# Performance work log

Measured on AMD Instinct MI355X. Metric: run time of the kernel, lower is better.

## Reference

```python
import jax, jax.numpy as jnp
import numpy as np

N = 20000   # nodes per graph
E = 320000  # edges per graph
D_IN, D_H = 128, 304


def _param(key, shape, fan_in):
    return jax.random.normal(key, shape, dtype=jnp.float32) / np.sqrt(fan_in)


def setup_inputs() -> dict:
    key = jax.random.key(0)
    ks = jax.random.split(key, 20)
    inp = {}
    for i, name in enumerate(['x1', 'x2', 'x3']):
        inp[name] = jax.random.normal(ks[i], (N, D_IN), dtype=jnp.float32)
    for i, name in enumerate(['src1', 'dst1', 'src2', 'dst2', 'src3', 'dst3']):
        inp[name] = jax.random.randint(ks[3 + i], (E,), 0, N, dtype=jnp.int32)
    # shared GraphConv weights (DGL GraphConv: h = norm_agg(x) @ W + b)
    inp['W1'] = _param(ks[9], (D_IN, D_H), D_IN)
    inp['b1'] = jnp.zeros((D_H,), jnp.float32)
    inp['W2'] = _param(ks[10], (D_H, D_H), D_H)
    inp['b2'] = jnp.zeros((D_H,), jnp.float32)
    inp['W3'] = _param(ks[11], (D_H, D_H), D_H)
    inp['b3'] = jnp.zeros((D_H,), jnp.float32)
    # MLP head: 304 -> 128 -> 64 -> 1
    inp['fW1'] = _param(ks[12], (D_H, 128), D_H)
    inp['fb1'] = jnp.zeros((128,), jnp.float32)
    inp['fW2'] = _param(ks[13], (128, 64), 128)
    inp['fb2'] = jnp.zeros((64,), jnp.float32)
    inp['fW3'] = _param(ks[14], (64, 1), 64)
    inp['fb3'] = jnp.zeros((1,), jnp.float32)
    return inp


def gcn_conv(x, src, dst, W, b):
    # DGL GraphConv, norm='both': h = D_in^{-1/2} A D_out^{-1/2} x W + b
    ones = jnp.ones((src.shape[0],), x.dtype)
    out_deg = jnp.clip(jax.ops.segment_sum(ones, src, num_segments=N), 1.0)
    in_deg = jnp.clip(jax.ops.segment_sum(ones, dst, num_segments=N), 1.0)
    h = x * jax.lax.rsqrt(out_deg)[:, None]
    agg = jax.ops.segment_sum(h[src], dst, num_segments=N)  # [N, d] SpMM
    agg = agg * jax.lax.rsqrt(in_deg)[:, None]
    return agg @ W + b


def reference(x1, x2, x3, src1, dst1, src2, dst2, src3, dst3,
              W1, b1, W2, b2, W3, b3, fW1, fb1, fW2, fb2, fW3, fb3):
    def branch(x, src, dst):
        x = jax.nn.relu(gcn_conv(x, src, dst, W1, b1))
        x = jax.nn.relu(gcn_conv(x, src, dst, W2, b2))
        x = jax.nn.relu(gcn_conv(x, src, dst, W3, b3))
        return x

    h1 = branch(x1, src1, dst1)
    h2 = branch(x2, src2, dst2)
    h3 = branch(x3, src3, dst3)
    # multi_graph_opt='max': max over all nodes of all three graphs -> [304]
    pooled = jnp.max(jnp.concatenate([h1, h2, h3], axis=0), axis=0)
    # output_opt='fc': MLP head with sigmoid
    z = jax.nn.relu(pooled @ fW1 + fb1)
    z = jax.nn.relu(z @ fW2 + fb2)
    return jax.nn.sigmoid(z @ fW3 + fb3)  # shape [1]
```

## Files before the change

kernel.cpp:

```cpp
#include <hip/hip_runtime.h>
#include <hip/hip_bf16.h>
#include <math.h>

#define NODES 20000
#define EDGES 320000
#define NB 3
#define TOTN (NODES * NB)
#define TOTE (EDGES * NB)
#define D_IN 128
#define D_H 304
#define SCAN_B 59
#define SLICES 40
#define SLICE_E (EDGES / SLICES)
#define ZX TOTN
#define ZQ (TOTN + 96)
#define OFFB 237
#define PACKB 7500
#define PREPWB 912

typedef __attribute__((ext_vector_type(4))) float f32x4;
typedef __attribute__((ext_vector_type(2))) float f32x2;

__device__ __forceinline__ void gload16(const void* g, void* l) {
    __builtin_amdgcn_global_load_lds(
        (const __attribute__((address_space(1))) unsigned*)g,
        (__attribute__((address_space(3))) unsigned*)l, 16, 0, 0);
}

__global__ __launch_bounds__(256, 1) void k_hist(
    const int* __restrict__ s1, const int* __restrict__ d1,
    const int* __restrict__ s2, const int* __restrict__ d2,
    const int* __restrict__ s3, const int* __restrict__ d3,
    unsigned short* __restrict__ partial_in, unsigned short* __restrict__ partial_out,
    int* __restrict__ gctr) {
    __shared__ unsigned hist[NODES / 2];
    if (blockIdx.x == 0 && blockIdx.y == 0 && threadIdx.x == 0) *gctr = 0;
    int g = blockIdx.x / SLICES, s = blockIdx.x % SLICES;
    bool isOut = (blockIdx.y == 1);
    const int* ep;
    if (isOut) ep = (g == 0) ? s1 : ((g == 1) ? s2 : s3);
    else       ep = (g == 0) ? d1 : ((g == 1) ? d2 : d3);
    ep += s * SLICE_E;
    for (int i = threadIdx.x; i < NODES / 2; i += 256) hist[i] = 0;
    __syncthreads();
    const int4* ep4 = (const int4*)ep;
    for (int i = threadIdx.x; i < SLICE_E / 4; i += 256) {
        int4 v = ep4[i];
        atomicAdd(&hist[v.x >> 1], 1u << ((v.x & 1) << 4));
        atomicAdd(&hist[v.y >> 1], 1u << ((v.y & 1) << 4));
        atomicAdd(&hist[v.z >> 1], 1u << ((v.z & 1) << 4));
        atomicAdd(&hist[v.w >> 1], 1u << ((v.w & 1) << 4));
    }
    __syncthreads();
    unsigned* po = (unsigned*)((isOut ? partial_out : partial_in) + (size_t)blockIdx.x * NODES);
    for (int i = threadIdx.x; i < NODES / 2; i += 256) po[i] = hist[i];
}

__global__ void k_degscan(const unsigned short* __restrict__ partial_in,
                          const unsigned short* __restrict__ partial_out,
                          float* __restrict__ inv_in, float* __restrict__ inv_out,
                          int* __restrict__ row_ptr, int* __restrict__ rend,
                          int* __restrict__ gctr) {
    __shared__ int wsum[16];
    __shared__ int sbase;
    int b = blockIdx.x, t = threadIdx.x;
    int i = b * 1024 + t;
    int lane = t & 63, wid = t >> 6;
    int v = 0;
    if (i < TOTN) {
        int g = i / NODES, ln = i - g * NODES;
        const unsigned short* pi = partial_in + (size_t)g * SLICES * NODES + ln;
        const unsigned short* po = partial_out + (size_t)g * SLICES * NODES + ln;
        int ci = 0, co = 0;
        #pragma unroll
        for (int s = 0; s < SLICES; s++) { ci += pi[s * NODES]; co += po[s * NODES]; }
        v = ci;
        inv_in[i]  = 1.0f / sqrtf((float)max(ci, 1));
        inv_out[i] = 1.0f / sqrtf((float)max(co, 1));
    }
    int sv = v;
    #pragma unroll
    for (int o = 1; o < 64; o <<= 1) {
        int u = __shfl_up(sv, o, 64);
        if (lane >= o) sv += u;
    }
    if (lane == 63) wsum[wid] = sv;
    __syncthreads();
    if (t < 16) {
        int w = wsum[t];
        #pragma unroll
        for (int o = 1; o < 16; o <<= 1) {
            int u = __shfl_up(w, o, 16);
            if (t >= o) w += u;
        }
        wsum[t] = w;
    }
    __syncthreads();
    if (t == 0) sbase = atomicAdd(gctr, wsum[15]);
    __syncthreads();
    int wbase = (wid > 0) ? wsum[wid - 1] : 0;
    if (i < TOTN) {
        int rp = sbase + wbase + sv - v;
        row_ptr[i] = rp;
        rend[i] = rp + v;
    }
}

__global__ void k_prep(const int* __restrict__ row_ptr,
                       const unsigned short* __restrict__ partial_in,
                       int* __restrict__ O,
                       int* __restrict__ csr_slack, unsigned* __restrict__ x8z,
                       unsigned* __restrict__ q8z, int* __restrict__ pooled,
                       const float4* __restrict__ x1, const float4* __restrict__ x2,
                       const float4* __restrict__ x3, const float* __restrict__ inv_out,
                       unsigned* __restrict__ q,
                       const float* __restrict__ W1, const float* __restrict__ W2,
                       const float* __restrict__ W3,
                       unsigned char* __restrict__ Wt1, unsigned char* __restrict__ Wt2,
                       unsigned char* __restrict__ Wt3) {
    if (blockIdx.x < OFFB) {
        int n = blockIdx.x * 256 + threadIdx.x;
        if (n >= TOTN) {
            int ex = n - TOTN;
            if (ex < 32) csr_slack[ex] = 0;
            else if (ex < 64) x8z[ex - 32] = 0;
            else if (ex < 144) q8z[ex - 64] = 0;
            else if (ex < 464) pooled[ex - 144] = 0;
            return;
        }
        int rp = row_ptr[n];
        int g = n / NODES, ln = n - g * NODES;
        const unsigned short* pi = partial_in + (size_t)g * SLICES * NODES + ln;
        int* on = O + (size_t)g * SLICES * NODES + ln;
        int run = rp;
        #pragma unroll
        for (int s = 0; s < SLICES; s++) {
            on[s * NODES] = run;
            run += pi[s * NODES];
        }
    } else if (blockIdx.x < OFFB + PACKB) {
        const int per = NODES * D_IN / 4;
        int i = (blockIdx.x - OFFB) * 256 + threadIdx.x;
        const float4* s; int j;
        if (i < per)          { s = x1; j = i; }
        else if (i < 2 * per) { s = x2; j = i - per; }
        else                  { s = x3; j = i - 2 * per; }
        float4 v = s[j];
        float sc = inv_out[i >> 5];
        int p = __builtin_amdgcn_cvt_pk_fp8_f32(v.x * sc, v.y * sc, 0, false);
        p = __builtin_amdgcn_cvt_pk_fp8_f32(v.z * sc, v.w * sc, p, true);
        q[i] = (unsigned)p;
    } else {
        const int N1 = D_H * 128, N2 = D_H * 320;
        int id = (blockIdx.x - OFFB - PACKB) * 256 + threadIdx.x;
        const float* W; unsigned char* Wt; int K, Kpad, lid;
        if (id < N1)                { W = W1; Wt = Wt1; K = 128; Kpad = 128; lid = id; }
        else if (id < N1 + N2)      { W = W2; Wt = Wt2; K = 304; Kpad = 320; lid = id - N1; }
        else                        { W = W3; Wt = Wt3; K = 304; Kpad = 320; lid = id - N1 - N2; }
        int n = lid / Kpad, k = lid - n * Kpad;
        unsigned char v = 0;
        if (k < K) {
            float w = W[k * D_H + n];
            v = (unsigned char)(__builtin_amdgcn_cvt_pk_fp8_f32(w, w, 0, false) & 0xff);
        }
        Wt[lid] = v;
    }
}

__global__ __launch_bounds__(256, 1) void k_fill2(
    const int* __restrict__ s1, const int* __restrict__ d1,
    const int* __restrict__ s2, const int* __restrict__ d2,
    const int* __restrict__ s3, const int* __restrict__ d3,
    const int* __restrict__ O, int* __restrict__ csr) {
    __shared__ int cur[NODES];
    int g = blockIdx.x / SLICES, s = blockIdx.x % SLICES;
    const int* sp = (g == 0) ? s1 : ((g == 1) ? s2 : s3);
    const int* dp = (g == 0) ? d1 : ((g == 1) ? d2 : d3);
    sp += s * SLICE_E; dp += s * SLICE_E;
    const int* on = O + (size_t)blockIdx.x * NODES;
    for (int i = threadIdx.x; i < NODES; i += 256) cur[i] = on[i];
    __syncthreads();
    int base = g * NODES;
    const int4* sp4 = (const int4*)sp;
    const int4* dp4 = (const int4*)dp;
    for (int i = threadIdx.x; i < SLICE_E / 4; i += 256) {
        int4 dv = dp4[i];
        int4 sv = sp4[i];
        int p0 = atomicAdd(&cur[dv.x], 1); csr[p0] = sv.x + base;
        int p1 = atomicAdd(&cur[dv.y], 1); csr[p1] = sv.y + base;
        int p2 = atomicAdd(&cur[dv.z], 1); csr[p2] = sv.z + base;
        int p3 = atomicAdd(&cur[dv.w], 1); csr[p3] = sv.w + base;
    }
}

__global__ void k_spmm_l1(const uint2* __restrict__ h, unsigned char* __restrict__ agg,
                          const int* __restrict__ row_ptr, const int* __restrict__ rend,
                          const int* __restrict__ csr,
                          const float* __restrict__ inv_in) {
    int n = blockIdx.x * 4 + (threadIdx.x >> 6);
    int lane = threadIdx.x & 63;
    int s = lane >> 4;
    int off = lane & 15;
    f32x2 a[4];
    #pragma unroll
    for (int j = 0; j < 4; j++) a[j] = (f32x2){0.f, 0.f};
    int k0 = row_ptr[n], k1 = rend[n];
    int deg = k1 - k0;
    const int* cp = csr + k0 + s;
    int e[8];
    #pragma unroll
    for (int j = 0; j < 8; j++) {
        int ev = cp[4 * j];
        e[j] = (s + 4 * j < deg) ? ev : ZX;
    }
    uint2 u[8];
    #pragma unroll
    for (int j = 0; j < 8; j++)
        if (4 * j < deg) u[j] = h[(size_t)e[j] * 16 + off];
    #pragma unroll
    for (int j = 0; j < 8; j++) {
        if (4 * j < deg) {
            a[0] += __builtin_amdgcn_cvt_pk_f32_fp8(u[j].x, false);
            a[1] += __builtin_amdgcn_cvt_pk_f32_fp8(u[j].x, true);
            a[2] += __builtin_amdgcn_cvt_pk_f32_fp8(u[j].y, false);
            a[3] += __builtin_amdgcn_cvt_pk_f32_fp8(u[j].y, true);
        }
    }
    for (int k = k0 + 32 + s; k < k1; k += 4) {
        int e0 = csr[k];
        uint2 u0 = h[(size_t)e0 * 16 + off];
        a[0] += __builtin_amdgcn_cvt_pk_f32_fp8(u0.x, false);
        a[1] += __builtin_amdgcn_cvt_pk_f32_fp8(u0.x, true);
        a[2] += __builtin_amdgcn_cvt_pk_f32_fp8(u0.y, false);
        a[3] += __builtin_amdgcn_cvt_pk_f32_fp8(u0.y, true);
    }
    float r[8];
    #pragma unroll
    for (int j = 0; j < 4; j++) {
        #pragma unroll
        for (int c = 0; c < 2; c++) {
            float v = a[j][c];
            r[2 * j + c] = v + __shfl(v, lane + 16, 64)
                             + __shfl(v, lane + 32, 64)
                             + __shfl(v, lane + 48, 64);
        }
    }
    if (lane < 16) {
        float wi = inv_in[n];
        int d0 = __builtin_amdgcn_cvt_pk_fp8_f32(r[0] * wi, r[1] * wi, 0, false);
        d0 = __builtin_amdgcn_cvt_pk_fp8_f32(r[2] * wi, r[3] * wi, d0, true);
        int d1 = __builtin_amdgcn_cvt_pk_fp8_f32(r[4] * wi, r[5] * wi, 0, false);
        d1 = __builtin_amdgcn_cvt_pk_fp8_f32(r[6] * wi, r[7] * wi, d1, true);
        uint2 st; st.x = (unsigned)d0; st.y = (unsigned)d1;
        *(uint2*)(agg + (size_t)n * 128 + lane * 8) = st;
    }
}

__global__ void k_spmm_big(const uint4* __restrict__ h, unsigned char* __restrict__ agg,
                           const int* __restrict__ row_ptr, const int* __restrict__ rend,
                           const int* __restrict__ csr,
                           const float* __restrict__ inv_in) {
    int n = blockIdx.x * 4 + (threadIdx.x >> 6);
    int lane = threadIdx.x & 63;
    int s = lane / 20;
    int off = lane % 20;
    f32x2 a[8];
    #pragma unroll
    for (int j = 0; j < 8; j++) a[j] = (f32x2){0.f, 0.f};
    int k0 = row_ptr[n], k1 = rend[n];
    int deg = k1 - k0;
    int degg = (s < 3) ? deg : 0;
    const int* cp = csr + k0 + s;
    int e[8];
    #pragma unroll
    for (int j = 0; j < 8; j++) {
        int ev = cp[3 * j];
        e[j] = (s + 3 * j < degg) ? ev : ZQ;
    }
    uint4 u[8];
    #pragma unroll
    for (int j = 0; j < 8; j++)
        if (3 * j < deg) u[j] = h[(size_t)e[j] * 20 + off];
    #pragma unroll
    for (int j = 0; j < 8; j++) {
        if (3 * j < deg) {
            a[0] += __builtin_amdgcn_cvt_pk_f32_fp8(u[j].x, false);
            a[1] += __builtin_amdgcn_cvt_pk_f32_fp8(u[j].x, true);
            a[2] += __builtin_amdgcn_cvt_pk_f32_fp8(u[j].y, false);
            a[3] += __builtin_amdgcn_cvt_pk_f32_fp8(u[j].y, true);
            a[4] += __builtin_amdgcn_cvt_pk_f32_fp8(u[j].z, false);
            a[5] += __builtin_amdgcn_cvt_pk_f32_fp8(u[j].z, true);
            a[6] += __builtin_amdgcn_cvt_pk_f32_fp8(u[j].w, false);
            a[7] += __builtin_amdgcn_cvt_pk_f32_fp8(u[j].w, true);
        }
    }
    int k1g = k0 + degg;
    for (int k = k0 + 24 + s; k < k1g; k += 3) {
        int e0 = csr[k];
        uint4 u0 = h[(size_t)e0 * 20 + off];
        a[0] += __builtin_amdgcn_cvt_pk_f32_fp8(u0.x, false);
        a[1] += __builtin_amdgcn_cvt_pk_f32_fp8(u0.x, true);
        a[2] += __builtin_amdgcn_cvt_pk_f32_fp8(u0.y, false);
        a[3] += __builtin_amdgcn_cvt_pk_f32_fp8(u0.y, true);
        a[4] += __builtin_amdgcn_cvt_pk_f32_fp8(u0.z, false);
        a[5] += __builtin_amdgcn_cvt_pk_f32_fp8(u0.z, true);
        a[6] += __builtin_amdgcn_cvt_pk_f32_fp8(u0.w, false);
        a[7] += __builtin_amdgcn_cvt_pk_f32_fp8(u0.w, true);
    }
    float r[16];
    #pragma unroll
    for (int j = 0; j < 8; j++) {
        #pragma unroll
        for (int c = 0; c < 2; c++) {
            float v = a[j][c];
            r[2 * j + c] = v + __shfl(v, lane + 20, 64) + __shfl(v, lane + 40, 64);
        }
    }
    if (lane < 20) {
        float wi = inv_in[n];
        int d0 = __builtin_amdgcn_cvt_pk_fp8_f32(r[0] * wi, r[1] * wi, 0, false);
        d0 = __builtin_amdgcn_cvt_pk_fp8_f32(r[2] * wi, r[3] * wi, d0, true);
        int d1 = __builtin_amdgcn_cvt_pk_fp8_f32(r[4] * wi, r[5] * wi, 0, false);
        d1 = __builtin_amdgcn_cvt_pk_fp8_f32(r[6] * wi, r[7] * wi, d1, true);
        int d2 = __builtin_amdgcn_cvt_pk_fp8_f32(r[8] * wi, r[9] * wi, 0, false);
        d2 = __builtin_amdgcn_cvt_pk_fp8_f32(r[10] * wi, r[11] * wi, d2, true);
        int d3 = __builtin_amdgcn_cvt_pk_fp8_f32(r[12] * wi, r[13] * wi, 0, false);
        d3 = __builtin_amdgcn_cvt_pk_fp8_f32(r[14] * wi, r[15] * wi, d3, true);
        uint4 st; st.x = (unsigned)d0; st.y = (unsigned)d1; st.z = (unsigned)d2; st.w = (unsigned)d3;
        *(uint4*)(agg + (size_t)n * 320 + lane * 16) = st;
    }
}

template <int MODE>
__global__ __launch_bounds__(256, 2) void k_gemm_mfma(
    const unsigned char* __restrict__ A, int lda,
    const unsigned char* __restrict__ Wt,
    const float* __restrict__ bias,
    const float* __restrict__ inv_out,
    unsigned char* __restrict__ C8, int* __restrict__ gpool, int M, int K) {
    __shared__ char SM[55296];
    __shared__ int pmax[D_H];
    int tid = threadIdx.x;
    int wv = tid >> 6, lane = tid & 63;
    int quad = lane >> 4, lrow = lane & 15;
    int bm = blockIdx.x * 128;

    if (MODE == 1) {
        for (int i = tid; i < D_H; i += 256) pmax[i] = 0;
    }

    f32x4 acc[2][19];
    #pragma unroll
    for (int r = 0; r < 2; r++)
        #pragma unroll
        for (int t = 0; t < 19; t++) acc[r][t] = (f32x4){0.f, 0.f, 0.f, 0.f};

    int swz = (lrow & 3) ^ (lrow >> 2);
    int hb = (quad & 1) * 8;

    auto stage = [&](int buf, int kt) {
        char* As = SM + buf * 27648;
        char* Bs = As + 8192;
        #pragma unroll
        for (int j = 0; j < 2; j++) {
            int c = j * 256 + tid;
            int row = c >> 2, xc = c & 3;
            int col = xc ^ (row & 3) ^ ((row >> 2) & 3);
            gload16(A + (size_t)(bm + row) * lda + kt + col * 16, As + c * 16);
        }
        #pragma unroll
        for (int j = 0; j < 5; j++) {
            int c = j * 256 + tid;
            if (c < 1216) {
                int row = c >> 2, xc = c & 3;
                int col = xc ^ (row & 3) ^ ((row >> 2) & 3);
                gload16(Wt + (size_t)row * K + kt + col * 16, Bs + c * 16);
            }
        }
    };

    int nt = K >> 6;
    stage(0, 0);
    __syncthreads();
    for (int t = 0; t < nt; t++) {
        if (t + 1 < nt) stage((t + 1) & 1, (t + 1) << 6);
        const char* As = SM + (t & 1) * 27648;
        const char* Bs = As + 8192;
        #pragma unroll
        for (int sub = 0; sub < 2; sub++) {
            int c0 = sub * 2 + (quad >> 1);
            int cx = (c0 ^ swz) * 16 + hb;
            int ra = wv * 32 + lrow;
            long long a0 = *(const long long*)(As + ra * 64 + cx);
            long long a1 = *(const long long*)(As + (ra + 16) * 64 + cx);
            #pragma unroll
            for (int u = 0; u < 19; u++) {
                long long b = *(const long long*)(Bs + (u * 16 + lrow) * 64 + cx);
                acc[0][u] = __builtin_amdgcn_mfma_f32_16x16x32_fp8_fp8(a0, b, acc[0][u], 0, 0, 0);
                acc[1][u] = __builtin_amdgcn_mfma_f32_16x16x32_fp8_fp8(a1, b, acc[1][u], 0, 0, 0);
            }
        }
        __syncthreads();
    }
    if (MODE == 0) {
        unsigned char* OUT = (unsigned char*)SM;
        if (tid < 128) *(uint4*)(OUT + tid * 320 + 304) = make_uint4(0u, 0u, 0u, 0u);
        #pragma unroll
        for (int t = 0; t < 19; t++) {
            int col = t * 16 + lrow;
            float bv = bias[col];
            #pragma unroll
            for (int r = 0; r < 2; r++) {
                int rl = wv * 32 + r * 16 + quad * 4;
                #pragma unroll
                for (int g = 0; g < 4; g++) {
                    int row = bm + rl + g;
                    float sc = inv_out[min(row, M - 1)];
                    float v = fmaxf(acc[r][t][g] + bv, 0.f) * sc;
                    int p = __builtin_amdgcn_cvt_pk_fp8_f32(v, v, 0, false);
                    OUT[(rl + g) * 320 + col] = (unsigned char)(p & 0xff);
                }
            }
        }
        __syncthreads();
        #pragma unroll
        for (int j = 0; j < 10; j++) {
            int c = j * 256 + tid;
            *(uint4*)(C8 + (size_t)bm * 320 + (size_t)c * 16) = *(const uint4*)(OUT + c * 16);
        }
    } else {
        #pragma unroll
        for (int t = 0; t < 19; t++) {
            int col = t * 16 + lrow;
            float bv = bias[col];
            float m = 0.f;
            #pragma unroll
            for (int r = 0; r < 2; r++) {
                int rbase = bm + wv * 32 + r * 16 + quad * 4;
                #pragma unroll
                for (int g = 0; g < 4; g++) {
                    int row = rbase + g;
                    if (row < M) m = fmaxf(m, fmaxf(acc[r][t][g] + bv, 0.f));
                }
            }
            atomicMax(&pmax[col], __float_as_int(m));
        }
        __syncthreads();
        for (int i = tid; i < D_H; i += 256)
            atomicMax(&gpool[i], pmax[i]);
    }
}

__global__ void k_mlp(const int* __restrict__ pooled_i,
                      const float* __restrict__ fW1, const float* __restrict__ fb1,
                      const float* __restrict__ fW2, const float* __restrict__ fb2,
                      const float* __restrict__ fW3, const float* __restrict__ fb3,
                      float* __restrict__ out) {
    __shared__ float p[D_H];
    __shared__ float z1[128];
    __shared__ float z2[64];
    int t = threadIdx.x;
    if (t < D_H) p[t] = __int_as_float(pooled_i[t]);
    __syncthreads();
    if (t < 128) {
        float acc = fb1[t];
        for (int k = 0; k < D_H; k++) acc += p[k] * fW1[k * 128 + t];
        z1[t] = fmaxf(acc, 0.f);
    }
    __syncthreads();
    if (t < 64) {
        float acc = fb2[t];
        for (int k = 0; k < 128; k++) acc += z1[k] * fW2[k * 64 + t];
        z2[t] = fmaxf(acc, 0.f);
    }
    __syncthreads();
    if (t == 0) {
        float acc = fb3[0];
        for (int k = 0; k < 64; k++) acc += z2[k] * fW3[k];
        out[0] = 1.f / (1.f + expf(-acc));
    }
}

extern "C" void kernel_launch(void* const* d_in, const int* in_sizes, int n_in,
                              void* d_out, int out_size, void* d_ws, size_t ws_size,
                              hipStream_t stream) {
    const float* x1 = (const float*)d_in[0];
    const float* x2 = (const float*)d_in[1];
    const float* x3 = (const float*)d_in[2];
    const int* src1 = (const int*)d_in[3];
    const int* dst1 = (const int*)d_in[4];
    const int* src2 = (const int*)d_in[5];
    const int* dst2 = (const int*)d_in[6];
    const int* src3 = (const int*)d_in[7];
    const int* dst3 = (const int*)d_in[8];
    const float* W1 = (const float*)d_in[9];
    const float* b1 = (const float*)d_in[10];
    const float* W2 = (const float*)d_in[11];
    const float* b2 = (const float*)d_in[12];
    const float* W3 = (const float*)d_in[13];
    const float* b3 = (const float*)d_in[14];
    const float* fW1 = (const float*)d_in[15];
    const float* fb1 = (const float*)d_in[16];
    const float* fW2 = (const float*)d_in[17];
    const float* fb2 = (const float*)d_in[18];
    const float* fW3 = (const float*)d_in[19];
    const float* fb3 = (const float*)d_in[20];
    float* out = (float*)d_out;

    char* w = (char*)d_ws;
    unsigned* X8       = (unsigned*)w;      w += (size_t)(TOTN + 1) * 32 * 4;
    unsigned char* Q8  = (unsigned char*)w; w += (size_t)(TOTN + 128) * 320;
    unsigned char* P8  = (unsigned char*)w; w += (size_t)(TOTN + 128) * 320;
    unsigned char* Wt1 = (unsigned char*)w; w += (size_t)D_H * 128;
    unsigned char* Wt2 = (unsigned char*)w; w += (size_t)D_H * 320;
    unsigned char* Wt3 = (unsigned char*)w; w += (size_t)D_H * 320;
    w = (char*)(((size_t)w + 255) & ~(size_t)255);
    unsigned short* partial_in  = (unsigned short*)w; w += (size_t)NB * SLICES * NODES * 2;
    unsigned short* partial_out = (unsigned short*)w; w += (size_t)NB * SLICES * NODES * 2;
    int* O         = (int*)w;    w += (size_t)NB * SLICES * NODES * 4;
    float* inv_out = (float*)w;  w += (size_t)TOTN * 4;
    float* inv_in  = (float*)w;  w += (size_t)TOTN * 4;
    int* row_ptr   = (int*)w;    w += (size_t)TOTN * 4;
    int* rend      = (int*)w;    w += (size_t)TOTN * 4;
    int* csr       = (int*)w;    w += (size_t)(TOTE + 32) * 4;
    int* pooled    = (int*)w;    w += 320 * 4;
    int* gctr      = (int*)w;    w += 64;

    k_hist<<<dim3(NB * SLICES, 2), 256, 0, stream>>>(src1, dst1, src2, dst2, src3, dst3,
                                                     partial_in, partial_out, gctr);
    k_degscan<<<SCAN_B, 1024, 0, stream>>>(partial_in, partial_out,
                                           inv_in, inv_out, row_ptr, rend, gctr);
    k_prep<<<OFFB + PACKB + PREPWB, 256, 0, stream>>>(
        row_ptr, partial_in, O, csr + TOTE,
        X8 + (size_t)ZX * 32, (unsigned*)(Q8 + (size_t)ZQ * 320), pooled,
        (const float4*)x1, (const float4*)x2, (const float4*)x3, inv_out, X8,
        W1, W2, W3, Wt1, Wt2, Wt3);
    k_fill2<<<NB * SLICES, 256, 0, stream>>>(src1, dst1, src2, dst2, src3, dst3, O, csr);

    int ggrid = (TOTN + 127) / 128;

    k_spmm_l1<<<TOTN / 4, 256, 0, stream>>>((const uint2*)X8, P8, row_ptr, rend, csr, inv_in);
    k_gemm_mfma<0><<<ggrid, 256, 0, stream>>>(P8, 128, Wt1, b1, inv_out,
                                              Q8, nullptr, TOTN, 128);
    k_spmm_big<<<TOTN / 4, 256, 0, stream>>>((const uint4*)Q8, P8, row_ptr, rend, csr, inv_in);
    k_gemm_mfma<0><<<ggrid, 256, 0, stream>>>(P8, 320, Wt2, b2, inv_out,
                                              Q8, nullptr, TOTN, 320);
    k_spmm_big<<<TOTN / 4, 256, 0, stream>>>((const uint4*)Q8, P8, row_ptr, rend, csr, inv_in);
    k_gemm_mfma<1><<<ggrid, 256, 0, stream>>>(P8, 320, Wt3, b3, nullptr,
                                              nullptr, pooled, TOTN, 320);

    k_mlp<<<1, 320, 0, stream>>>(pooled, fW1, fb1, fW2, fb2, fW3, fb3, out);
}
```

Measured before the change: 322.5 us.

## Fold slice offsets into degscan, widen hist/fill blocks, pad weight tiles

Per-slice CSR offset computation moves from k_prep into k_degscan, which removes one dependent pass over row_ptr. k_hist and k_fill2 now run 1024-thread blocks instead of 256, giving more wavefronts to hide latency in the atomic-heavy histogram and scatter loops. Transposed fp8 weights are padded to 320 rows so the GEMM staging loop drops its bounds check, at the cost of a larger LDS buffer. Zero-fill of slack buffers moves to a single trailing block in k_prep.

Measured after the change: 317.0 us. Within noise of the previous version (-1.7%).

```diff
diff --git a/kernel.cpp b/kernel.cpp
--- a/kernel.cpp
+++ b/kernel.cpp
@@ -14,9 +14,8 @@
 #define SLICE_E (EDGES / SLICES)
 #define ZX TOTN
 #define ZQ (TOTN + 96)
-#define OFFB 237
 #define PACKB 7500
-#define PREPWB 912
+#define PREPWB 960
 
 typedef __attribute__((ext_vector_type(4))) float f32x4;
 typedef __attribute__((ext_vector_type(2))) float f32x2;
@@ -27,7 +26,7 @@
         (__attribute__((address_space(3))) unsigned*)l, 16, 0, 0);
 }
 
-__global__ __launch_bounds__(256, 1) void k_hist(
+__global__ __launch_bounds__(1024, 1) void k_hist(
     const int* __restrict__ s1, const int* __restrict__ d1,
     const int* __restrict__ s2, const int* __restrict__ d2,
     const int* __restrict__ s3, const int* __restrict__ d3,
@@ -41,10 +40,10 @@
     if (isOut) ep = (g == 0) ? s1 : ((g == 1) ? s2 : s3);
     else       ep = (g == 0) ? d1 : ((g == 1) ? d2 : d3);
     ep += s * SLICE_E;
-    for (int i = threadIdx.x; i < NODES / 2; i += 256) hist[i] = 0;
+    for (int i = threadIdx.x; i < NODES / 2; i += 1024) hist[i] = 0;
     __syncthreads();
     const int4* ep4 = (const int4*)ep;
-    for (int i = threadIdx.x; i < SLICE_E / 4; i += 256) {
+    for (int i = threadIdx.x; i < SLICE_E / 4; i += 1024) {
         int4 v = ep4[i];
         atomicAdd(&hist[v.x >> 1], 1u << ((v.x & 1) << 4));
         atomicAdd(&hist[v.y >> 1], 1u << ((v.y & 1) << 4));
@@ -53,22 +52,23 @@
     }
     __syncthreads();
     unsigned* po = (unsigned*)((isOut ? partial_out : partial_in) + (size_t)blockIdx.x * NODES);
-    for (int i = threadIdx.x; i < NODES / 2; i += 256) po[i] = hist[i];
+    for (int i = threadIdx.x; i < NODES / 2; i += 1024) po[i] = hist[i];
 }
 
 __global__ void k_degscan(const unsigned short* __restrict__ partial_in,
                           const unsigned short* __restrict__ partial_out,
                           float* __restrict__ inv_in, float* __restrict__ inv_out,
                           int* __restrict__ row_ptr, int* __restrict__ rend,
-                          int* __restrict__ gctr) {
+                          int* __restrict__ O, int* __restrict__ gctr) {
     __shared__ int wsum[16];
     __shared__ int sbase;
     int b = blockIdx.x, t = threadIdx.x;
     int i = b * 1024 + t;
     int lane = t & 63, wid = t >> 6;
     int v = 0;
+    int g = 0, ln = 0;
     if (i < TOTN) {
-        int g = i / NODES, ln = i - g * NODES;
+        g = i / NODES; ln = i - g * NODES;
         const unsigned short* pi = partial_in + (size_t)g * SLICES * NODES + ln;
         const unsigned short* po = partial_out + (size_t)g * SLICES * NODES + ln;
         int ci = 0, co = 0;
@@ -103,44 +103,29 @@
         int rp = sbase + wbase + sv - v;
         row_ptr[i] = rp;
         rend[i] = rp + v;
-    }
-}
-
-__global__ void k_prep(const int* __restrict__ row_ptr,
-                       const unsigned short* __restrict__ partial_in,
-                       int* __restrict__ O,
-                       int* __restrict__ csr_slack, unsigned* __restrict__ x8z,
-                       unsigned* __restrict__ q8z, int* __restrict__ pooled,
-                       const float4* __restrict__ x1, const float4* __restrict__ x2,
+        const unsigned short* pi = partial_in + (size_t)g * SLICES * NODES + ln;
+        int* on = O + (size_t)g * SLICES * NODES + ln;
+        int run = rp;
+        #pragma unroll
+        for (int s = 0; s < SLICES; s++) {
+            on[s * NODES] = run;
+            run += pi[s * NODES];
+        }
+    }
+}
+
+__global__ void k_prep(const float4* __restrict__ x1, const float4* __restrict__ x2,
                        const float4* __restrict__ x3, const float* __restrict__ inv_out,
                        unsigned* __restrict__ q,
                        const float* __restrict__ W1, const float* __restrict__ W2,
                        const float* __restrict__ W3,
                        unsigned char* __restrict__ Wt1, unsigned char* __restrict__ Wt2,
-                       unsigned char* __restrict__ Wt3) {
-    if (blockIdx.x < OFFB) {
-        int n = blockIdx.x * 256 + threadIdx.x;
-        if (n >= TOTN) {
-            int ex = n - TOTN;
-            if (ex < 32) csr_slack[ex] = 0;
-            else if (ex < 64) x8z[ex - 32] = 0;
-            else if (ex < 144) q8z[ex - 64] = 0;
-            else if (ex < 464) pooled[ex - 144] = 0;
-            return;
-        }
-        int rp = row_ptr[n];
-        int g = n / NODES, ln = n - g * NODES;
-        const unsigned short* pi = partial_in + (size_t)g * SLICES * NODES + ln;
-        int* on = O + (size_t)g * SLICES * NODES + ln;
-        int run = rp;
-        #pragma unroll
-        for (int s = 0; s < SLICES; s++) {
-            on[s * NODES] = run;
-            run += pi[s * NODES];
-        }
-    } else if (blockIdx.x < OFFB + PACKB) {
+                       unsigned char* __restrict__ Wt3,
+                       int* __restrict__ csr_slack, unsigned* __restrict__ x8z,
+                       unsigned* __restrict__ q8z, int* __restrict__ pooled) {
+    if (blockIdx.x < PACKB) {
         const int per = NODES * D_IN / 4;
-        int i = (blockIdx.x - OFFB) * 256 + threadIdx.x;
+        int i = blockIdx.x * 256 + threadIdx.x;
         const float4* s; int j;
         if (i < per)          { s = x1; j = i; }
         else if (i < 2 * per) { s = x2; j = i - per; }
@@ -150,24 +135,30 @@
         int p = __builtin_amdgcn_cvt_pk_fp8_f32(v.x * sc, v.y * sc, 0, false);
         p = __builtin_amdgcn_cvt_pk_fp8_f32(v.z * sc, v.w * sc, p, true);
         q[i] = (unsigned)p;
-    } else {
-        const int N1 = D_H * 128, N2 = D_H * 320;
-        int id = (blockIdx.x - OFFB - PACKB) * 256 + threadIdx.x;
+    } else if (blockIdx.x < PACKB + PREPWB) {
+        const int N1 = 320 * 128, N2 = 320 * 320;
+        int id = (blockIdx.x - PACKB) * 256 + threadIdx.x;
         const float* W; unsigned char* Wt; int K, Kpad, lid;
         if (id < N1)                { W = W1; Wt = Wt1; K = 128; Kpad = 128; lid = id; }
         else if (id < N1 + N2)      { W = W2; Wt = Wt2; K = 304; Kpad = 320; lid = id - N1; }
         else                        { W = W3; Wt = Wt3; K = 304; Kpad = 320; lid = id - N1 - N2; }
         int n = lid / Kpad, k = lid - n * Kpad;
         unsigned char v = 0;
-        if (k < K) {
+        if (k < K && n < D_H) {
             float w = W[k * D_H + n];
             v = (unsigned char)(__builtin_amdgcn_cvt_pk_fp8_f32(w, w, 0, false) & 0xff);
         }
         Wt[lid] = v;
-    }
-}
-
-__global__ __launch_bounds__(256, 1) void k_fill2(
+    } else {
+        int ex = threadIdx.x;
+        if (ex < 32) csr_slack[ex] = 0;
+        else if (ex < 64) x8z[ex - 32] = 0;
+        else if (ex < 144) q8z[ex - 64] = 0;
+        else if (ex < 464) pooled[ex - 144] = 0;
+    }
+}
+
+__global__ __launch_bounds__(1024, 1) void k_fill2(
     const int* __restrict__ s1, const int* __restrict__ d1,
     const int* __restrict__ s2, const int* __restrict__ d2,
     const int* __restrict__ s3, const int* __restrict__ d3,
@@ -178,12 +169,12 @@
     const int* dp = (g == 0) ? d1 : ((g == 1) ? d2 : d3);
     sp += s * SLICE_E; dp += s * SLICE_E;
     const int* on = O + (size_t)blockIdx.x * NODES;
-    for (int i = threadIdx.x; i < NODES; i += 256) cur[i] = on[i];
+    for (int i = threadIdx.x; i < NODES; i += 1024) cur[i] = on[i];
     __syncthreads();
     int base = g * NODES;
     const int4* sp4 = (const int4*)sp;
     const int4* dp4 = (const int4*)dp;
-    for (int i = threadIdx.x; i < SLICE_E / 4; i += 256) {
+    for (int i = threadIdx.x; i < SLICE_E / 4; i += 1024) {
         int4 dv = dp4[i];
         int4 sv = sp4[i];
         int p0 = atomicAdd(&cur[dv.x], 1); csr[p0] = sv.x + base;
@@ -338,7 +329,7 @@
     const float* __restrict__ bias,
     const float* __restrict__ inv_out,
     unsigned char* __restrict__ C8, int* __restrict__ gpool, int M, int K) {
-    __shared__ char SM[55296];
+    __shared__ char SM[57344];
     __shared__ int pmax[D_H];
     int tid = threadIdx.x;
     int wv = tid >> 6, lane = tid & 63;
@@ -359,7 +350,7 @@
     int hb = (quad & 1) * 8;
 
     auto stage = [&](int buf, int kt) {
-        char* As = SM + buf * 27648;
+        char* As = SM + buf * 28672;
         char* Bs = As + 8192;
         #pragma unroll
         for (int j = 0; j < 2; j++) {
@@ -371,11 +362,9 @@
         #pragma unroll
         for (int j = 0; j < 5; j++) {
             int c = j * 256 + tid;
-            if (c < 1216) {
-                int row = c >> 2, xc = c & 3;
-                int col = xc ^ (row & 3) ^ ((row >> 2) & 3);
-                gload16(Wt + (size_t)row * K + kt + col * 16, Bs + c * 16);
-            }
+            int row = c >> 2, xc = c & 3;
+            int col = xc ^ (row & 3) ^ ((row >> 2) & 3);
+            gload16(Wt + (size_t)row * K + kt + col * 16, Bs + c * 16);
         }
     };
 
@@ -384,7 +373,7 @@
     __syncthreads();
     for (int t = 0; t < nt; t++) {
         if (t + 1 < nt) stage((t + 1) & 1, (t + 1) << 6);
-        const char* As = SM + (t & 1) * 27648;
+        const char* As = SM + (t & 1) * 28672;
         const char* Bs = As + 8192;
         #pragma unroll
         for (int sub = 0; sub < 2; sub++) {
@@ -511,9 +500,9 @@
     unsigned* X8       = (unsigned*)w;      w += (size_t)(TOTN + 1) * 32 * 4;
     unsigned char* Q8  = (unsigned char*)w; w += (size_t)(TOTN + 128) * 320;
     unsigned char* P8  = (unsigned char*)w; w += (size_t)(TOTN + 128) * 320;
-    unsigned char* Wt1 = (unsigned char*)w; w += (size_t)D_H * 128;
-    unsigned char* Wt2 = (unsigned char*)w; w += (size_t)D_H * 320;
-    unsigned char* Wt3 = (unsigned char*)w; w += (size_t)D_H * 320;
+    unsigned char* Wt1 = (unsigned char*)w; w += (size_t)320 * 128;
+    unsigned char* Wt2 = (unsigned char*)w; w += (size_t)320 * 320;
+    unsigned char* Wt3 = (unsigned char*)w; w += (size_t)320 * 320;
     w = (char*)(((size_t)w + 255) & ~(size_t)255);
     unsigned short* partial_in  = (unsigned short*)w; w += (size_t)NB * SLICES * NODES * 2;
     unsigned short* partial_out = (unsigned short*)w; w += (size_t)NB * SLICES * NODES * 2;
@@ -526,16 +515,15 @@
     int* pooled    = (int*)w;    w += 320 * 4;
     int* gctr      = (int*)w;    w += 64;
 
-    k_hist<<<dim3(NB * SLICES, 2), 256, 0, stream>>>(src1, dst1, src2, dst2, src3, dst3,
-                                                     partial_in, partial_out, gctr);
+    k_hist<<<dim3(NB * SLICES, 2), 1024, 0, stream>>>(src1, dst1, src2, dst2, src3, dst3,
+                                                      partial_in, partial_out, gctr);
     k_degscan<<<SCAN_B, 1024, 0, stream>>>(partial_in, partial_out,
-                                           inv_in, inv_out, row_ptr, rend, gctr);
-    k_prep<<<OFFB + PACKB + PREPWB, 256, 0, stream>>>(
-        row_ptr, partial_in, O, csr + TOTE,
-        X8 + (size_t)ZX * 32, (unsigned*)(Q8 + (size_t)ZQ * 320), pooled,
+                                           inv_in, inv_out, row_ptr, rend, O, gctr);
+    k_prep<<<PACKB + PREPWB + 1, 256, 0, stream>>>(
         (const float4*)x1, (const float4*)x2, (const float4*)x3, inv_out, X8,
-        W1, W2, W3, Wt1, Wt2, Wt3);
-    k_fill2<<<NB * SLICES, 256, 0, stream>>>(src1, dst1, src2, dst2, src3, dst3, O, csr);
+        W1, W2, W3, Wt1, Wt2, Wt3,
+        csr + TOTE, X8 + (size_t)ZX * 32, (unsigned*)(Q8 + (size_t)ZQ * 320), pooled);
+    k_fill2<<<NB * SLICES, 1024, 0, stream>>>(src1, dst1, src2, dst2, src3, dst3, O, csr);
 
     int ggrid = (TOTN + 127) / 128;
 
```
